# Optimization experiments

Measured on AMD Instinct MI355X. Metric: run time of the kernel, lower is better.

The kernel has to match this reference:

```python
import jax, jax.numpy as jnp
import numpy as np
import math

D = 128
LAMBDA_INIT = 0.8 - 0.6 * math.exp(-0.3 * 1)  # depth=1


def _clin(xr, xi, wr, wi, br, bi):
    # complex linear: (xr + i xi) @ (wr + i wi)^T + (br + i bi)
    o_r = jnp.einsum('bhsd,od->bhso', xr, wr) - jnp.einsum('bhsd,od->bhso', xi, wi) + br
    o_i = jnp.einsum('bhsd,od->bhso', xr, wi) + jnp.einsum('bhsd,od->bhso', xi, wr) + bi
    return o_r, o_i


def setup_inputs() -> dict:
    key = jax.random.key(0)
    ks = jax.random.split(key, 32)
    B, H, S = 1, 12, 1024
    shp = (B, H, S, D)
    inp = {}
    names = ['q_r', 'q_i', 'k_r', 'k_i', 'v_r', 'v_i', 'pe_q_r', 'pe_q_i', 'pe_k_r', 'pe_k_i']
    for i, n in enumerate(names):
        inp[n] = jax.random.normal(ks[i], shp, dtype=jnp.float32)
    std = 1.0 / math.sqrt(D)
    inp['qw_r'] = jax.random.normal(ks[10], (2 * D, D), jnp.float32) * std
    inp['qw_i'] = jax.random.normal(ks[11], (2 * D, D), jnp.float32) * std
    inp['qb_r'] = jnp.zeros((2 * D,), jnp.float32)
    inp['qb_i'] = jnp.zeros((2 * D,), jnp.float32)
    for j, p in enumerate(['k', 'v', 'g', 'o']):
        inp[p + 'w_r'] = jax.random.normal(ks[12 + 2 * j], (D, D), jnp.float32) * std
        inp[p + 'w_i'] = jax.random.normal(ks[13 + 2 * j], (D, D), jnp.float32) * std
        inp[p + 'b_r'] = jnp.zeros((D,), jnp.float32)
        inp[p + 'b_i'] = jnp.zeros((D,), jnp.float32)
    inp['lq1'] = jax.random.normal(ks[20], (D,), jnp.float32) * 0.1
    inp['lk1'] = jax.random.normal(ks[21], (D,), jnp.float32) * 0.1
    inp['lq2'] = jax.random.normal(ks[22], (D,), jnp.float32) * 0.1
    inp['lk2'] = jax.random.normal(ks[23], (D,), jnp.float32) * 0.1
    inp['sub_w'] = jnp.ones((2 * D,), jnp.float32)
    return inp


def _forward(q_r, q_i, k_r, k_i, v_r, v_i, pe_q_r, pe_q_i, pe_k_r, pe_k_i,
             qw_r, qw_i, qb_r, qb_i, kw_r, kw_i, kb_r, kb_i,
             vw_r, vw_i, vb_r, vb_i, gw_r, gw_i, gb_r, gb_i,
             ow_r, ow_i, ob_r, ob_i, lq1, lk1, lq2, lk2, sub_w):
    scale = D ** (-0.5)
    qp_r, qp_i = _clin(q_r, q_i, qw_r, qw_i, qb_r, qb_i)   # [B,H,S,2D]
    kp_r, kp_i = _clin(k_r, k_i, kw_r, kw_i, kb_r, kb_i)   # [B,H,S,D]
    vp_r, vp_i = _clin(v_r, v_i, vw_r, vw_i, vb_r, vb_i)
    qp_r = qp_r + jnp.concatenate([pe_q_r, pe_q_r], axis=-1)
    qp_i = qp_i + jnp.concatenate([pe_q_i, pe_q_i], axis=-1)
    kp_r = kp_r + pe_k_r
    kp_i = kp_i + pe_k_i
    q1_r, q2_r = jnp.split(qp_r, 2, axis=-1)
    q1_i, q2_i = jnp.split(qp_i, 2, axis=-1)

    def attn_w(qr, qi):
        s_r = jnp.einsum('bhqd,bhkd->bhqk', qr, kp_r) + jnp.einsum('bhqd,bhkd->bhqk', qi, kp_i)
        s_i = jnp.einsum('bhqd,bhkd->bhqk', qi, kp_r) - jnp.einsum('bhqd,bhkd->bhqk', qr, kp_i)
        mag = jnp.sqrt(s_r ** 2 + s_i ** 2 + 1e-8) * scale
        return jax.nn.softmax(mag.astype(jnp.float32), axis=-1).astype(s_r.dtype)

    w1 = attn_w(q1_r, q1_i)
    w2 = attn_w(q2_r, q2_i)
    a1_r = jnp.einsum('bhqk,bhkd->bhqd', w1, vp_r)
    a1_i = jnp.einsum('bhqk,bhkd->bhqd', w1, vp_i)
    a2_r = jnp.einsum('bhqk,bhkd->bhqd', w2, vp_r)
    a2_i = jnp.einsum('bhqk,bhkd->bhqd', w2, vp_i)
    cat_r = jnp.concatenate([a1_r, a2_r], axis=-1)
    cat_i = jnp.concatenate([a1_i, a2_i], axis=-1)
    rms = jnp.sqrt(jnp.mean(cat_r ** 2 + cat_i ** 2, axis=-1, keepdims=True) + 1e-5)
    cat_r = cat_r / rms * sub_w
    cat_i = cat_i / rms * sub_w
    a1_r, a2_r = jnp.split(cat_r, 2, axis=-1)
    a1_i, a2_i = jnp.split(cat_i, 2, axis=-1)
    lam1 = jnp.exp(jnp.sum(lq1 * lk1))
    lam2 = jnp.exp(jnp.sum(lq2 * lk2))
    lam = jax.nn.sigmoid(lam1 - lam2 + LAMBDA_INIT)
    out_r = a1_r - lam * a2_r
    out_i = a1_i - lam * a2_i
    g_r, g_i = _clin(q_r, q_i, gw_r, gw_i, gb_r, gb_i)
    out_r, out_i = g_r * out_r - g_i * out_i, g_r * out_i + g_i * out_r
    out_r, out_i = _clin(out_r, out_i, ow_r, ow_i, ob_r, ob_i)
    return out_r, out_i


def reference(q_r, q_i, k_r, k_i, v_r, v_i, pe_q_r, pe_q_i, pe_k_r, pe_k_i,
              qw_r, qw_i, qb_r, qb_i, kw_r, kw_i, kb_r, kb_i,
              vw_r, vw_i, vb_r, vb_i, gw_r, gw_i, gb_r, gb_i,
              ow_r, ow_i, ob_r, ob_i, lq1, lk1, lq2, lk2, sub_w):
    return _forward(q_r, q_i, k_r, k_i, v_r, v_i, pe_q_r, pe_q_i, pe_k_r, pe_k_i,
                    qw_r, qw_i, qb_r, qb_i, kw_r, kw_i, kb_r, kb_i,
                    vw_r, vw_i, vb_r, vb_i, gw_r, gw_i, gb_r, gb_i,
                    ow_r, ow_i, ob_r, ob_i, lq1, lk1, lq2, lk2, sub_w)
```

## Files before the change

### kernel.cpp

```cpp
#include <hip/hip_runtime.h>
#include <math.h>

#define H 12
#define S 1024
#define D 128
#define NROWS (H * S)

typedef __attribute__((ext_vector_type(8))) _Float16 f16x8;
typedef __attribute__((ext_vector_type(4))) float f32x4;
typedef __attribute__((ext_vector_type(4))) int i32x4;

__device__ __forceinline__ short f2h(float f) {
    _Float16 h = (_Float16)f;
    return __builtin_bit_cast(short, h);
}
__device__ __forceinline__ f16x8 fneg8(f16x8 v) {
    i32x4 u = __builtin_bit_cast(i32x4, v);
    u ^= (int)0x80008000;
    return __builtin_bit_cast(f16x8, u);
}

#define WS_QP_R   0ULL
#define WS_QP_I   6291456ULL
#define WS_KP_R   12582912ULL
#define WS_KP_I   15728640ULL
#define WS_VPT_R  18874368ULL
#define WS_VPT_I  22020096ULL
#define WS_G_R    25165824ULL
#define WS_G_I    31457280ULL
#define WS_ACAT_R 37748736ULL
#define WS_ACAT_I 50331648ULL
#define WS_LAM    62914560ULL
#define WS_SC     62914816ULL
#define W16_PER_HEAD  4194304ULL

__global__ void lam_kernel(const float* __restrict__ lq1, const float* __restrict__ lk1,
                           const float* __restrict__ lq2, const float* __restrict__ lk2,
                           float* __restrict__ lam_out)
{
    int t = threadIdx.x;
    float p1 = lq1[t] * lk1[t];
    float p2 = lq2[t] * lk2[t];
    #pragma unroll
    for (int off = 32; off; off >>= 1) {
        p1 += __shfl_xor(p1, off);
        p2 += __shfl_xor(p2, off);
    }
    __shared__ float s1[2], s2[2];
    if ((t & 63) == 0) { s1[t >> 6] = p1; s2[t >> 6] = p2; }
    __syncthreads();
    if (t == 0) {
        float l1 = expf(s1[0] + s1[1]);
        float l2 = expf(s2[0] + s2[1]);
        float x = l1 - l2 + 0.3555090675909693f;
        lam_out[0] = 1.0f / (1.0f + expf(-x));
    }
}

template <int OMODE>
__global__ __launch_bounds__(256) void clin_mfma(
    const float* __restrict__ xr, const float* __restrict__ xi,
    const float* __restrict__ wr, const float* __restrict__ wi,
    const float* __restrict__ br, const float* __restrict__ bi,
    const float* __restrict__ per, const float* __restrict__ pei,
    void* __restrict__ outr_, void* __restrict__ outi_, int M)
{
    __shared__ short As[64 * 72], Brs[64 * 72], Bis[64 * 72];
    const int t = threadIdx.x;
    const int row0 = blockIdx.x * 64, col0 = blockIdx.y * 64;
    const int lane = t & 63, wid = t >> 6;
    const int wm = (wid >> 1) * 32, wn = (wid & 1) * 32;
    const int fm = lane & 15, fq = lane >> 4;
    f32x4 zero4 = {0.f, 0.f, 0.f, 0.f};
    f32x4 accr[2][2], acci[2][2];
    #pragma unroll
    for (int i = 0; i < 2; ++i)
        #pragma unroll
        for (int j = 0; j < 2; ++j) { accr[i][j] = zero4; acci[i][j] = zero4; }

    for (int c = 0; c < 4; ++c) {
        const bool hi = (c >= 2);
        const int kb = (c & 1) * 64;
        const float* Asrc = hi ? xi : xr;
        const float* Brsrc = hi ? wi : wr;
        const float* Bisrc = hi ? wr : wi;
        const float bsign = hi ? -1.0f : 1.0f;
        __syncthreads();
        #pragma unroll
        for (int i = 0; i < 4; ++i) {
            int lin = i * 256 + t;
            int r = lin >> 4;
            int k4 = (lin & 15) * 4;
            float4 va = *(const float4*)&Asrc[(size_t)(row0 + r) * 128 + kb + k4];
            *(short4*)&As[r * 72 + k4] = make_short4(f2h(va.x), f2h(va.y), f2h(va.z), f2h(va.w));
            float4 vr = *(const float4*)&Brsrc[(size_t)(col0 + r) * 128 + kb + k4];
            *(short4*)&Brs[r * 72 + k4] = make_short4(f2h(bsign * vr.x), f2h(bsign * vr.y),
                                                      f2h(bsign * vr.z), f2h(bsign * vr.w));
            float4 vi = *(const float4*)&Bisrc[(size_t)(col0 + r) * 128 + kb + k4];
            *(short4*)&Bis[r * 72 + k4] = make_short4(f2h(vi.x), f2h(vi.y), f2h(vi.z), f2h(vi.w));
        }
        __syncthreads();
        #pragma unroll
        for (int ks = 0; ks < 64; ks += 32) {
            f16x8 a[2], bfr[2], bfi[2];
            #pragma unroll
            for (int i = 0; i < 2; ++i) {
                a[i]   = *(const f16x8*)&As[(wm + i * 16 + fm) * 72 + ks + fq * 8];
                bfr[i] = *(const f16x8*)&Brs[(wn + i * 16 + fm) * 72 + ks + fq * 8];
                bfi[i] = *(const f16x8*)&Bis[(wn + i * 16 + fm) * 72 + ks + fq * 8];
            }
            #pragma unroll
            for (int i = 0; i < 2; ++i)
                #pragma unroll
                for (int j = 0; j < 2; ++j) {
                    accr[i][j] = __builtin_amdgcn_mfma_f32_16x16x32_f16(a[i], bfr[j], accr[i][j], 0, 0, 0);
                    acci[i][j] = __builtin_amdgcn_mfma_f32_16x16x32_f16(a[i], bfi[j], acci[i][j], 0, 0, 0);
                }
        }
    }
    #pragma unroll
    for (int i = 0; i < 2; ++i)
        #pragma unroll
        for (int j = 0; j < 2; ++j) {
            int colc = col0 + wn + j * 16 + fm;
            float bbr = br[colc], bbi = bi[colc];
            if (OMODE == 2) {
                int rb = row0 + wm + i * 16 + fq * 4;
                int hq = rb >> 10, sq = rb & 1023;
                short4 o_r4, o_i4;
                float r0 = accr[i][j][0] + bbr, r1 = accr[i][j][1] + bbr;
                float r2 = accr[i][j][2] + bbr, r3 = accr[i][j][3] + bbr;
                float i0 = acci[i][j][0] + bbi, i1 = acci[i][j][1] + bbi;
                float i2v = acci[i][j][2] + bbi, i3 = acci[i][j][3] + bbi;
                o_r4 = make_short4(f2h(r0), f2h(r1), f2h(r2), f2h(r3));
                o_i4 = make_short4(f2h(i0), f2h(i1), f2h(i2v), f2h(i3));
                size_t ob = ((size_t)(hq * 128 + colc)) * 1024 + sq;
                *(short4*)&((short*)outr_)[ob] = o_r4;
                *(short4*)&((short*)outi_)[ob] = o_i4;
            } else {
                #pragma unroll
                for (int reg = 0; reg < 4; ++reg) {
                    int rr = row0 + wm + i * 16 + fq * 4 + reg;
                    float o_r = accr[i][j][reg] + bbr;
                    float o_i = acci[i][j][reg] + bbi;
                    if (per) {
                        o_r += per[(size_t)rr * 128 + (colc & 127)];
                        o_i += pei[(size_t)rr * 128 + (colc & 127)];
                    }
                    if (OMODE == 1) {
                        ((short*)outr_)[(size_t)rr * M + colc] = f2h(o_r);
                        ((short*)outi_)[(size_t)rr * M + colc] = f2h(o_i);
                    } else {
                        ((float*)outr_)[(size_t)rr * M + colc] = o_r;
                        ((float*)outi_)[(size_t)rr * M + colc] = o_i;
                    }
                }
            }
        }
}

__global__ __launch_bounds__(256) void score_mfma(
    const short* __restrict__ qp_r, const short* __restrict__ qp_i,
    const short* __restrict__ kp_r, const short* __restrict__ kp_i,
    short* __restrict__ w16, int h0)
{
    __shared__ short Qr[64 * 72], Qi[64 * 72], Kt[128 * 72];
    const int t = threadIdx.x;
    const int hh = blockIdx.z >> 1, map = blockIdx.z & 1;
    const int h = h0 + hh;
    const int q0 = blockIdx.x * 64, c0 = blockIdx.y * 128;
    const int lane = t & 63, wid = t >> 6;
    const int wm = (wid >> 1) * 32, wn = (wid & 1) * 64;
    const int fm = lane & 15, fq = lane >> 4;
    f32x4 zero4 = {0.f, 0.f, 0.f, 0.f};
    f32x4 sr[2][4], si[2][4];
    #pragma unroll
    for (int i = 0; i < 2; ++i)
        #pragma unroll
        for (int j = 0; j < 4; ++j) { sr[i][j] = zero4; si[i][j] = zero4; }

    for (int kb = 0; kb < 2; ++kb) {
        const int kbase = map * 128 + kb * 64;
        __syncthreads();
        #pragma unroll
        for (int i = 0; i < 4; ++i) {
            int lin = i * 256 + t;
            int r = lin >> 4, k4 = (lin & 15) * 4;
            size_t qb = (size_t)(h * S + q0 + r) * 256 + kbase + k4;
            *(short4*)&Qr[r * 72 + k4] = *(const short4*)&qp_r[qb];
            *(short4*)&Qi[r * 72 + k4] = *(const short4*)&qp_i[qb];
        }
        #pragma unroll
        for (int i = 0; i < 8; ++i) {
            int lin = i * 256 + t;
            int r = lin >> 4, k4 = (lin & 15) * 4;
            *(short4*)&Kt[r * 72 + k4] =
                *(const short4*)&kp_r[(size_t)(h * S + c0 + r) * 128 + kb * 64 + k4];
        }
        __syncthreads();
        f16x8 aR[2][2], aI[2][2];
        #pragma unroll
        for (int ks = 0; ks < 2; ++ks)
            #pragma unroll
            for (int i = 0; i < 2; ++i) {
                int ao = (wm + i * 16 + fm) * 72 + ks * 32 + fq * 8;
                aR[ks][i] = *(const f16x8*)&Qr[ao];
                aI[ks][i] = *(const f16x8*)&Qi[ao];
            }
        #pragma unroll
        for (int ks = 0; ks < 2; ++ks) {
            f16x8 b[4];
            #pragma unroll
            for (int j = 0; j < 4; ++j)
                b[j] = *(const f16x8*)&Kt[(wn + j * 16 + fm) * 72 + ks * 32 + fq * 8];
            #pragma unroll
            for (int i = 0; i < 2; ++i)
                #pragma unroll
                for (int j = 0; j < 4; ++j) {
                    sr[i][j] = __builtin_amdgcn_mfma_f32_16x16x32_f16(aR[ks][i], b[j], sr[i][j], 0, 0, 0);
                    si[i][j] = __builtin_amdgcn_mfma_f32_16x16x32_f16(aI[ks][i], b[j], si[i][j], 0, 0, 0);
                }
        }
        __syncthreads();
        #pragma unroll
        for (int i = 0; i < 8; ++i) {
            int lin = i * 256 + t;
            int r = lin >> 4, k4 = (lin & 15) * 4;
            *(short4*)&Kt[r * 72 + k4] =
                *(const short4*)&kp_i[(size_t)(h * S + c0 + r) * 128 + kb * 64 + k4];
        }
        __syncthreads();
        #pragma unroll
        for (int ks = 0; ks < 2; ++ks) {
            f16x8 b[4];
            #pragma unroll
            for (int j = 0; j < 4; ++j)
                b[j] = *(const f16x8*)&Kt[(wn + j * 16 + fm) * 72 + ks * 32 + fq * 8];
            f16x8 nR0 = fneg8(aR[ks][0]), nR1 = fneg8(aR[ks][1]);
            #pragma unroll
            for (int j = 0; j < 4; ++j) {
                sr[0][j] = __builtin_amdgcn_mfma_f32_16x16x32_f16(aI[ks][0], b[j], sr[0][j], 0, 0, 0);
                si[0][j] = __builtin_amdgcn_mfma_f32_16x16x32_f16(nR0, b[j], si[0][j], 0, 0, 0);
                sr[1][j] = __builtin_amdgcn_mfma_f32_16x16x32_f16(aI[ks][1], b[j], sr[1][j], 0, 0, 0);
                si[1][j] = __builtin_amdgcn_mfma_f32_16x16x32_f16(nR1, b[j], si[1][j], 0, 0, 0);
            }
        }
    }
    const float scale = 0.08838834764831845f;
    #pragma unroll
    for (int i = 0; i < 2; ++i)
        #pragma unroll
        for (int j = 0; j < 4; ++j) {
            int kcol = c0 + wn + j * 16 + fm;
            #pragma unroll
            for (int reg = 0; reg < 4; ++reg) {
                int q = q0 + wm + i * 16 + fq * 4 + reg;
                float r1 = sr[i][j][reg], I1 = si[i][j][reg];
                float m1 = sqrtf(fmaf(r1, r1, fmaf(I1, I1, 1e-8f))) * scale;
                w16[(((size_t)hh * 2 + map) * S + q) * S + kcol] = f2h(m1);
            }
        }
}

__global__ __launch_bounds__(256) void softmax_f16(short* __restrict__ w16)
{
    short* row = w16 + (size_t)blockIdx.x * S;
    int t = threadIdx.x;
    short4 s = ((short4*)row)[t];
    float f0 = (float)__builtin_bit_cast(_Float16, s.x);
    float f1 = (float)__builtin_bit_cast(_Float16, s.y);
    float f2v = (float)__builtin_bit_cast(_Float16, s.z);
    float f3 = (float)__builtin_bit_cast(_Float16, s.w);
    float m = fmaxf(fmaxf(f0, f1), fmaxf(f2v, f3));
    #pragma unroll
    for (int off = 32; off; off >>= 1) m = fmaxf(m, __shfl_xor(m, off));
    __shared__ float redm[4], reds[4];
    int w = t >> 6;
    if ((t & 63) == 0) redm[w] = m;
    __syncthreads();
    m = fmaxf(fmaxf(redm[0], redm[1]), fmaxf(redm[2], redm[3]));
    float e0 = __expf(f0 - m), e1 = __expf(f1 - m), e2 = __expf(f2v - m), e3 = __expf(f3 - m);
    float ssum = e0 + e1 + e2 + e3;
    #pragma unroll
    for (int off = 32; off; off >>= 1) ssum += __shfl_xor(ssum, off);
    if ((t & 63) == 0) reds[w] = ssum;
    __syncthreads();
    ssum = reds[0] + reds[1] + reds[2] + reds[3];
    float inv = 1.0f / ssum;
    s.x = f2h(e0 * inv); s.y = f2h(e1 * inv); s.z = f2h(e2 * inv); s.w = f2h(e3 * inv);
    ((short4*)row)[t] = s;
}

__global__ __launch_bounds__(256) void av_mfma(
    const short* __restrict__ w16, const short* __restrict__ vpT_r, const short* __restrict__ vpT_i,
    float* __restrict__ acat_r, float* __restrict__ acat_i, int h0)
{
    __shared__ short W1[64 * 72], W2[64 * 72], Vr[64 * 72], Vi[64 * 72];
    const int t = threadIdx.x;
    const int hh = blockIdx.z, h = h0 + hh;
    const int q0 = blockIdx.x * 64, d0 = blockIdx.y * 64;
    const int lane = t & 63, wid = t >> 6;
    const int wm = (wid >> 1) * 32, wn = (wid & 1) * 32;
    const int fm = lane & 15, fq = lane >> 4;
    f32x4 zero4 = {0.f, 0.f, 0.f, 0.f};
    f32x4 a1r[2][2], a1i[2][2], a2r[2][2], a2i[2][2];
    #pragma unroll
    for (int i = 0; i < 2; ++i)
        #pragma unroll
        for (int j = 0; j < 2; ++j) { a1r[i][j] = zero4; a1i[i][j] = zero4; a2r[i][j] = zero4; a2i[i][j] = zero4; }

    for (int k0 = 0; k0 < S; k0 += 64) {
        __syncthreads();
        #pragma unroll
        for (int i = 0; i < 4; ++i) {
            int lin = i * 256 + t;
            int r = lin >> 4, k4 = (lin & 15) * 4;
            *(short4*)&W1[r * 72 + k4] = *(const short4*)&w16[(((size_t)hh * 2 + 0) * S + q0 + r) * S + k0 + k4];
            *(short4*)&W2[r * 72 + k4] = *(const short4*)&w16[(((size_t)hh * 2 + 1) * S + q0 + r) * S + k0 + k4];
            size_t vb = (size_t)(h * 128 + d0 + r) * 1024 + k0 + k4;
            *(short4*)&Vr[r * 72 + k4] = *(const short4*)&vpT_r[vb];
            *(short4*)&Vi[r * 72 + k4] = *(const short4*)&vpT_i[vb];
        }
        __syncthreads();
        #pragma unroll
        for (int ks = 0; ks < 64; ks += 32) {
            f16x8 w1[2], w2[2], br[2], bi[2];
            #pragma unroll
            for (int i = 0; i < 2; ++i) {
                w1[i] = *(const f16x8*)&W1[(wm + i * 16 + fm) * 72 + ks + fq * 8];
                w2[i] = *(const f16x8*)&W2[(wm + i * 16 + fm) * 72 + ks + fq * 8];
                br[i] = *(const f16x8*)&Vr[(wn + i * 16 + fm) * 72 + ks + fq * 8];
                bi[i] = *(const f16x8*)&Vi[(wn + i * 16 + fm) * 72 + ks + fq * 8];
            }
            #pragma unroll
            for (int i = 0; i < 2; ++i)
                #pragma unroll
                for (int j = 0; j < 2; ++j) {
                    a1r[i][j] = __builtin_amdgcn_mfma_f32_16x16x32_f16(w1[i], br[j], a1r[i][j], 0, 0, 0);
                    a1i[i][j] = __builtin_amdgcn_mfma_f32_16x16x32_f16(w1[i], bi[j], a1i[i][j], 0, 0, 0);
                    a2r[i][j] = __builtin_amdgcn_mfma_f32_16x16x32_f16(w2[i], br[j], a2r[i][j], 0, 0, 0);
                    a2i[i][j] = __builtin_amdgcn_mfma_f32_16x16x32_f16(w2[i], bi[j], a2i[i][j], 0, 0, 0);
                }
        }
    }
    #pragma unroll
    for (int i = 0; i < 2; ++i)
        #pragma unroll
        for (int j = 0; j < 2; ++j) {
            int d = d0 + wn + j * 16 + fm;
            #pragma unroll
            for (int reg = 0; reg < 4; ++reg) {
                int q = q0 + wm + i * 16 + fq * 4 + reg;
                size_t rowb = (size_t)(h * S + q) * 256;
                acat_r[rowb + d]       = a1r[i][j][reg];
                acat_r[rowb + 128 + d] = a2r[i][j][reg];
                acat_i[rowb + d]       = a1i[i][j][reg];
                acat_i[rowb + 128 + d] = a2i[i][j][reg];
            }
        }
}

__global__ __launch_bounds__(256) void rmsgate_kernel(
    const float* __restrict__ acat_r, const float* __restrict__ acat_i,
    const float* __restrict__ sub_w, const float* __restrict__ lam_ptr,
    float* __restrict__ g_r, float* __restrict__ g_i)
{
    int row = blockIdx.x;
    int t = threadIdx.x;
    float ar = acat_r[(size_t)row * 256 + t];
    float ai = acat_i[(size_t)row * 256 + t];
    float ss = fmaf(ar, ar, ai * ai);
    #pragma unroll
    for (int off = 32; off; off >>= 1) ss += __shfl_xor(ss, off);
    __shared__ float red[4];
    if ((t & 63) == 0) red[t >> 6] = ss;
    __syncthreads();
    float total = red[0] + red[1] + red[2] + red[3];
    float inv_rms = 1.0f / sqrtf(total * (1.0f / 256.0f) + 1e-5f);
    float sw = sub_w[t];
    __shared__ float Cr[256], Ci[256];
    Cr[t] = ar * inv_rms * sw;
    Ci[t] = ai * inv_rms * sw;
    __syncthreads();
    if (t < 128) {
        float lam = lam_ptr[0];
        float o_r = Cr[t] - lam * Cr[t + 128];
        float o_i = Ci[t] - lam * Ci[t + 128];
        float gr = g_r[(size_t)row * 128 + t];
        float gi = g_i[(size_t)row * 128 + t];
        g_r[(size_t)row * 128 + t] = gr * o_r - gi * o_i;
        g_i[(size_t)row * 128 + t] = gr * o_i + gi * o_r;
    }
}

extern "C" void kernel_launch(void* const* d_in, const int* in_sizes, int n_in,
                              void* d_out, int out_size, void* d_ws, size_t ws_size,
                              hipStream_t stream)
{
    (void)in_sizes; (void)n_in; (void)out_size;
    const float* q_r    = (const float*)d_in[0];
    const float* q_i    = (const float*)d_in[1];
    const float* k_r    = (const float*)d_in[2];
    const float* k_i    = (const float*)d_in[3];
    const float* v_r    = (const float*)d_in[4];
    const float* v_i    = (const float*)d_in[5];
    const float* pe_q_r = (const float*)d_in[6];
    const float* pe_q_i = (const float*)d_in[7];
    const float* pe_k_r = (const float*)d_in[8];
    const float* pe_k_i = (const float*)d_in[9];
    const float* qw_r   = (const float*)d_in[10];
    const float* qw_i   = (const float*)d_in[11];
    const float* qb_r   = (const float*)d_in[12];
    const float* qb_i   = (const float*)d_in[13];
    const float* kw_r   = (const float*)d_in[14];
    const float* kw_i   = (const float*)d_in[15];
    const float* kb_r   = (const float*)d_in[16];
    const float* kb_i   = (const float*)d_in[17];
    const float* vw_r   = (const float*)d_in[18];
    const float* vw_i   = (const float*)d_in[19];
    const float* vb_r   = (const float*)d_in[20];
    const float* vb_i   = (const float*)d_in[21];
    const float* gw_r   = (const float*)d_in[22];
    const float* gw_i   = (const float*)d_in[23];
    const float* gb_r   = (const float*)d_in[24];
    const float* gb_i   = (const float*)d_in[25];
    const float* ow_r   = (const float*)d_in[26];
    const float* ow_i   = (const float*)d_in[27];
    const float* ob_r   = (const float*)d_in[28];
    const float* ob_i   = (const float*)d_in[29];
    const float* lq1    = (const float*)d_in[30];
    const float* lk1    = (const float*)d_in[31];
    const float* lq2    = (const float*)d_in[32];
    const float* lk2    = (const float*)d_in[33];
    const float* sub_w  = (const float*)d_in[34];

    char* ws = (char*)d_ws;
    short* qp_r   = (short*)(ws + WS_QP_R);
    short* qp_i   = (short*)(ws + WS_QP_I);
    short* kp_r   = (short*)(ws + WS_KP_R);
    short* kp_i   = (short*)(ws + WS_KP_I);
    short* vpT_r  = (short*)(ws + WS_VPT_R);
    short* vpT_i  = (short*)(ws + WS_VPT_I);
    float* g_r    = (float*)(ws + WS_G_R);
    float* g_i    = (float*)(ws + WS_G_I);
    float* acat_r = (float*)(ws + WS_ACAT_R);
    float* acat_i = (float*)(ws + WS_ACAT_I);
    float* lam    = (float*)(ws + WS_LAM);
    short* w16    = (short*)(ws + WS_SC);

    float* out_r = (float*)d_out;
    float* out_i = out_r + (size_t)NROWS * D;

    size_t avail = ws_size > WS_SC ? ws_size - WS_SC : 0;
    int nh_chunk = (int)(avail / W16_PER_HEAD);
    if (nh_chunk < 1) nh_chunk = 1;
    if (nh_chunk > H) nh_chunk = H;

    lam_kernel<<<1, 128, 0, stream>>>(lq1, lk1, lq2, lk2, lam);

    clin_mfma<1><<<dim3(192, 4), 256, 0, stream>>>(q_r, q_i, qw_r, qw_i, qb_r, qb_i,
                                                   pe_q_r, pe_q_i, qp_r, qp_i, 256);
    clin_mfma<1><<<dim3(192, 2), 256, 0, stream>>>(k_r, k_i, kw_r, kw_i, kb_r, kb_i,
                                                   pe_k_r, pe_k_i, kp_r, kp_i, 128);
    clin_mfma<2><<<dim3(192, 2), 256, 0, stream>>>(v_r, v_i, vw_r, vw_i, vb_r, vb_i,
                                                   nullptr, nullptr, vpT_r, vpT_i, 128);
    clin_mfma<0><<<dim3(192, 2), 256, 0, stream>>>(q_r, q_i, gw_r, gw_i, gb_r, gb_i,
                                                   nullptr, nullptr, g_r, g_i, 128);

    for (int h0 = 0; h0 < H; h0 += nh_chunk) {
        int nhh = (H - h0 < nh_chunk) ? (H - h0) : nh_chunk;
        score_mfma<<<dim3(16, 8, nhh * 2), 256, 0, stream>>>(qp_r, qp_i, kp_r, kp_i, w16, h0);
        softmax_f16<<<nhh * 2 * S, 256, 0, stream>>>(w16);
        av_mfma<<<dim3(16, 2, nhh), 256, 0, stream>>>(w16, vpT_r, vpT_i, acat_r, acat_i, h0);
    }

    rmsgate_kernel<<<NROWS, 256, 0, stream>>>(acat_r, acat_i, sub_w, lam, g_r, g_i);

    clin_mfma<0><<<dim3(192, 2), 256, 0, stream>>>(g_r, g_i, ow_r, ow_i, ob_r, ob_i,
                                                   nullptr, nullptr, out_r, out_i, 128);
}
```

Measured before the change: 320.1 us.

## Enlarge GEMM tiles and split AV kernel by complex component

The complex-linear and score kernels now use 128-row M tiles with 4x2 and 4x4 per-wave fragment grids. This halves the grid size and raises reuse of the shared B/K tile. The AV kernel now handles one complex component per block across all 128 output dims, so each W tile is reused across 128 columns, but the W tiles are loaded twice, once per component. The larger tiles use more registers and LDS, which can lower occupancy, and the smaller grids (96 or 192 blocks) may underfill the GPU's 256 CUs.

```diff
diff --git a/kernel.cpp b/kernel.cpp
--- a/kernel.cpp
+++ b/kernel.cpp
@@ -65,16 +65,16 @@
     const float* __restrict__ per, const float* __restrict__ pei,
     void* __restrict__ outr_, void* __restrict__ outi_, int M)
 {
-    __shared__ short As[64 * 72], Brs[64 * 72], Bis[64 * 72];
+    __shared__ short As[128 * 72], Brs[64 * 72], Bis[64 * 72];
     const int t = threadIdx.x;
-    const int row0 = blockIdx.x * 64, col0 = blockIdx.y * 64;
+    const int row0 = blockIdx.x * 128, col0 = blockIdx.y * 64;
     const int lane = t & 63, wid = t >> 6;
-    const int wm = (wid >> 1) * 32, wn = (wid & 1) * 32;
+    const int wm = (wid >> 1) * 64, wn = (wid & 1) * 32;
     const int fm = lane & 15, fq = lane >> 4;
     f32x4 zero4 = {0.f, 0.f, 0.f, 0.f};
-    f32x4 accr[2][2], acci[2][2];
-    #pragma unroll
-    for (int i = 0; i < 2; ++i)
+    f32x4 accr[4][2], acci[4][2];
+    #pragma unroll
+    for (int i = 0; i < 4; ++i)
         #pragma unroll
         for (int j = 0; j < 2; ++j) { accr[i][j] = zero4; acci[i][j] = zero4; }
 
@@ -87,12 +87,16 @@
         const float bsign = hi ? -1.0f : 1.0f;
         __syncthreads();
         #pragma unroll
-        for (int i = 0; i < 4; ++i) {
-            int lin = i * 256 + t;
-            int r = lin >> 4;
-            int k4 = (lin & 15) * 4;
+        for (int it = 0; it < 8; ++it) {
+            int lin = it * 256 + t;
+            int r = lin >> 4, k4 = (lin & 15) * 4;
             float4 va = *(const float4*)&Asrc[(size_t)(row0 + r) * 128 + kb + k4];
             *(short4*)&As[r * 72 + k4] = make_short4(f2h(va.x), f2h(va.y), f2h(va.z), f2h(va.w));
+        }
+        #pragma unroll
+        for (int it = 0; it < 4; ++it) {
+            int lin = it * 256 + t;
+            int r = lin >> 4, k4 = (lin & 15) * 4;
             float4 vr = *(const float4*)&Brsrc[(size_t)(col0 + r) * 128 + kb + k4];
             *(short4*)&Brs[r * 72 + k4] = make_short4(f2h(bsign * vr.x), f2h(bsign * vr.y),
                                                       f2h(bsign * vr.z), f2h(bsign * vr.w));
@@ -102,24 +106,25 @@
         __syncthreads();
         #pragma unroll
         for (int ks = 0; ks < 64; ks += 32) {
-            f16x8 a[2], bfr[2], bfi[2];
-            #pragma unroll
-            for (int i = 0; i < 2; ++i) {
-                a[i]   = *(const f16x8*)&As[(wm + i * 16 + fm) * 72 + ks + fq * 8];
-                bfr[i] = *(const f16x8*)&Brs[(wn + i * 16 + fm) * 72 + ks + fq * 8];
-                bfi[i] = *(const f16x8*)&Bis[(wn + i * 16 + fm) * 72 + ks + fq * 8];
-            }
-            #pragma unroll
-            for (int i = 0; i < 2; ++i)
+            f16x8 bfr[2], bfi[2];
+            #pragma unroll
+            for (int j = 0; j < 2; ++j) {
+                bfr[j] = *(const f16x8*)&Brs[(wn + j * 16 + fm) * 72 + ks + fq * 8];
+                bfi[j] = *(const f16x8*)&Bis[(wn + j * 16 + fm) * 72 + ks + fq * 8];
+            }
+            #pragma unroll
+            for (int i = 0; i < 4; ++i) {
+                f16x8 a = *(const f16x8*)&As[(wm + i * 16 + fm) * 72 + ks + fq * 8];
                 #pragma unroll
                 for (int j = 0; j < 2; ++j) {
-                    accr[i][j] = __builtin_amdgcn_mfma_f32_16x16x32_f16(a[i], bfr[j], accr[i][j], 0, 0, 0);
-                    acci[i][j] = __builtin_amdgcn_mfma_f32_16x16x32_f16(a[i], bfi[j], acci[i][j], 0, 0, 0);
+                    accr[i][j] = __builtin_amdgcn_mfma_f32_16x16x32_f16(a, bfr[j], accr[i][j], 0, 0, 0);
+                    acci[i][j] = __builtin_amdgcn_mfma_f32_16x16x32_f16(a, bfi[j], acci[i][j], 0, 0, 0);
                 }
-        }
-    }
-    #pragma unroll
-    for (int i = 0; i < 2; ++i)
+            }
+        }
+    }
+    #pragma unroll
+    for (int i = 0; i < 4; ++i)
         #pragma unroll
         for (int j = 0; j < 2; ++j) {
             int colc = col0 + wn + j * 16 + fm;
@@ -127,13 +132,10 @@
             if (OMODE == 2) {
                 int rb = row0 + wm + i * 16 + fq * 4;
                 int hq = rb >> 10, sq = rb & 1023;
-                short4 o_r4, o_i4;
-                float r0 = accr[i][j][0] + bbr, r1 = accr[i][j][1] + bbr;
-                float r2 = accr[i][j][2] + bbr, r3 = accr[i][j][3] + bbr;
-                float i0 = acci[i][j][0] + bbi, i1 = acci[i][j][1] + bbi;
-                float i2v = acci[i][j][2] + bbi, i3 = acci[i][j][3] + bbi;
-                o_r4 = make_short4(f2h(r0), f2h(r1), f2h(r2), f2h(r3));
-                o_i4 = make_short4(f2h(i0), f2h(i1), f2h(i2v), f2h(i3));
+                short4 o_r4 = make_short4(f2h(accr[i][j][0] + bbr), f2h(accr[i][j][1] + bbr),
+                                          f2h(accr[i][j][2] + bbr), f2h(accr[i][j][3] + bbr));
+                short4 o_i4 = make_short4(f2h(acci[i][j][0] + bbi), f2h(acci[i][j][1] + bbi),
+                                          f2h(acci[i][j][2] + bbi), f2h(acci[i][j][3] + bbi));
                 size_t ob = ((size_t)(hq * 128 + colc)) * 1024 + sq;
                 *(short4*)&((short*)outr_)[ob] = o_r4;
                 *(short4*)&((short*)outi_)[ob] = o_i4;
@@ -164,18 +166,18 @@
     const short* __restrict__ kp_r, const short* __restrict__ kp_i,
     short* __restrict__ w16, int h0)
 {
-    __shared__ short Qr[64 * 72], Qi[64 * 72], Kt[128 * 72];
+    __shared__ short Qr[128 * 72], Qi[128 * 72], Kt[128 * 72];
     const int t = threadIdx.x;
     const int hh = blockIdx.z >> 1, map = blockIdx.z & 1;
     const int h = h0 + hh;
-    const int q0 = blockIdx.x * 64, c0 = blockIdx.y * 128;
+    const int q0 = blockIdx.x * 128, c0 = blockIdx.y * 128;
     const int lane = t & 63, wid = t >> 6;
-    const int wm = (wid >> 1) * 32, wn = (wid & 1) * 64;
+    const int wm = (wid >> 1) * 64, wn = (wid & 1) * 64;
     const int fm = lane & 15, fq = lane >> 4;
     f32x4 zero4 = {0.f, 0.f, 0.f, 0.f};
-    f32x4 sr[2][4], si[2][4];
-    #pragma unroll
-    for (int i = 0; i < 2; ++i)
+    f32x4 sr[4][4], si[4][4];
+    #pragma unroll
+    for (int i = 0; i < 4; ++i)
         #pragma unroll
         for (int j = 0; j < 4; ++j) { sr[i][j] = zero4; si[i][j] = zero4; }
 
@@ -183,72 +185,66 @@
         const int kbase = map * 128 + kb * 64;
         __syncthreads();
         #pragma unroll
-        for (int i = 0; i < 4; ++i) {
-            int lin = i * 256 + t;
+        for (int it = 0; it < 8; ++it) {
+            int lin = it * 256 + t;
             int r = lin >> 4, k4 = (lin & 15) * 4;
             size_t qb = (size_t)(h * S + q0 + r) * 256 + kbase + k4;
             *(short4*)&Qr[r * 72 + k4] = *(const short4*)&qp_r[qb];
             *(short4*)&Qi[r * 72 + k4] = *(const short4*)&qp_i[qb];
-        }
-        #pragma unroll
-        for (int i = 0; i < 8; ++i) {
-            int lin = i * 256 + t;
-            int r = lin >> 4, k4 = (lin & 15) * 4;
             *(short4*)&Kt[r * 72 + k4] =
                 *(const short4*)&kp_r[(size_t)(h * S + c0 + r) * 128 + kb * 64 + k4];
         }
         __syncthreads();
-        f16x8 aR[2][2], aI[2][2];
-        #pragma unroll
-        for (int ks = 0; ks < 2; ++ks)
-            #pragma unroll
-            for (int i = 0; i < 2; ++i) {
-                int ao = (wm + i * 16 + fm) * 72 + ks * 32 + fq * 8;
-                aR[ks][i] = *(const f16x8*)&Qr[ao];
-                aI[ks][i] = *(const f16x8*)&Qi[ao];
-            }
-        #pragma unroll
-        for (int ks = 0; ks < 2; ++ks) {
+        #pragma unroll
+        for (int ks = 0; ks < 64; ks += 32) {
             f16x8 b[4];
             #pragma unroll
             for (int j = 0; j < 4; ++j)
-                b[j] = *(const f16x8*)&Kt[(wn + j * 16 + fm) * 72 + ks * 32 + fq * 8];
-            #pragma unroll
-            for (int i = 0; i < 2; ++i)
+                b[j] = *(const f16x8*)&Kt[(wn + j * 16 + fm) * 72 + ks + fq * 8];
+            #pragma unroll
+            for (int i = 0; i < 4; ++i) {
+                int ao = (wm + i * 16 + fm) * 72 + ks + fq * 8;
+                f16x8 ar = *(const f16x8*)&Qr[ao];
+                f16x8 ai = *(const f16x8*)&Qi[ao];
                 #pragma unroll
                 for (int j = 0; j < 4; ++j) {
-                    sr[i][j] = __builtin_amdgcn_mfma_f32_16x16x32_f16(aR[ks][i], b[j], sr[i][j], 0, 0, 0);
-                    si[i][j] = __builtin_amdgcn_mfma_f32_16x16x32_f16(aI[ks][i], b[j], si[i][j], 0, 0, 0);
+                    sr[i][j] = __builtin_amdgcn_mfma_f32_16x16x32_f16(ar, b[j], sr[i][j], 0, 0, 0);
+                    si[i][j] = __builtin_amdgcn_mfma_f32_16x16x32_f16(ai, b[j], si[i][j], 0, 0, 0);
                 }
-        }
-        __syncthreads();
-        #pragma unroll
-        for (int i = 0; i < 8; ++i) {
-            int lin = i * 256 + t;
+            }
+        }
+        __syncthreads();
+        #pragma unroll
+        for (int it = 0; it < 8; ++it) {
+            int lin = it * 256 + t;
             int r = lin >> 4, k4 = (lin & 15) * 4;
             *(short4*)&Kt[r * 72 + k4] =
                 *(const short4*)&kp_i[(size_t)(h * S + c0 + r) * 128 + kb * 64 + k4];
         }
         __syncthreads();
         #pragma unroll
-        for (int ks = 0; ks < 2; ++ks) {
+        for (int ks = 0; ks < 64; ks += 32) {
             f16x8 b[4];
             #pragma unroll
             for (int j = 0; j < 4; ++j)
-                b[j] = *(const f16x8*)&Kt[(wn + j * 16 + fm) * 72 + ks * 32 + fq * 8];
-            f16x8 nR0 = fneg8(aR[ks][0]), nR1 = fneg8(aR[ks][1]);
-            #pragma unroll
-            for (int j = 0; j < 4; ++j) {
-                sr[0][j] = __builtin_amdgcn_mfma_f32_16x16x32_f16(aI[ks][0], b[j], sr[0][j], 0, 0, 0);
-                si[0][j] = __builtin_amdgcn_mfma_f32_16x16x32_f16(nR0, b[j], si[0][j], 0, 0, 0);
-                sr[1][j] = __builtin_amdgcn_mfma_f32_16x16x32_f16(aI[ks][1], b[j], sr[1][j], 0, 0, 0);
-                si[1][j] = __builtin_amdgcn_mfma_f32_16x16x32_f16(nR1, b[j], si[1][j], 0, 0, 0);
+                b[j] = *(const f16x8*)&Kt[(wn + j * 16 + fm) * 72 + ks + fq * 8];
+            #pragma unroll
+            for (int i = 0; i < 4; ++i) {
+                int ao = (wm + i * 16 + fm) * 72 + ks + fq * 8;
+                f16x8 ar = *(const f16x8*)&Qr[ao];
+                f16x8 ai = *(const f16x8*)&Qi[ao];
+                f16x8 nr = fneg8(ar);
+                #pragma unroll
+                for (int j = 0; j < 4; ++j) {
+                    sr[i][j] = __builtin_amdgcn_mfma_f32_16x16x32_f16(ai, b[j], sr[i][j], 0, 0, 0);
+                    si[i][j] = __builtin_amdgcn_mfma_f32_16x16x32_f16(nr, b[j], si[i][j], 0, 0, 0);
+                }
             }
         }
     }
     const float scale = 0.08838834764831845f;
     #pragma unroll
-    for (int i = 0; i < 2; ++i)
+    for (int i = 0; i < 4; ++i)
         #pragma unroll
         for (int j = 0; j < 4; ++j) {
             int kcol = c0 + wn + j * 16 + fm;
@@ -295,67 +291,69 @@
     const short* __restrict__ w16, const short* __restrict__ vpT_r, const short* __restrict__ vpT_i,
     float* __restrict__ acat_r, float* __restrict__ acat_i, int h0)
 {
-    __shared__ short W1[64 * 72], W2[64 * 72], Vr[64 * 72], Vi[64 * 72];
+    __shared__ short W1[64 * 72], W2[64 * 72], Vc[128 * 72];
     const int t = threadIdx.x;
     const int hh = blockIdx.z, h = h0 + hh;
-    const int q0 = blockIdx.x * 64, d0 = blockIdx.y * 64;
+    const int comp = blockIdx.y;
+    const int q0 = blockIdx.x * 64;
+    const short* vpT = comp ? vpT_i : vpT_r;
+    float* acat = comp ? acat_i : acat_r;
     const int lane = t & 63, wid = t >> 6;
-    const int wm = (wid >> 1) * 32, wn = (wid & 1) * 32;
+    const int wm = (wid >> 1) * 32, wn = (wid & 1) * 64;
     const int fm = lane & 15, fq = lane >> 4;
     f32x4 zero4 = {0.f, 0.f, 0.f, 0.f};
-    f32x4 a1r[2][2], a1i[2][2], a2r[2][2], a2i[2][2];
+    f32x4 a1[2][4], a2[2][4];
     #pragma unroll
     for (int i = 0; i < 2; ++i)
         #pragma unroll
-        for (int j = 0; j < 2; ++j) { a1r[i][j] = zero4; a1i[i][j] = zero4; a2r[i][j] = zero4; a2i[i][j] = zero4; }
+        for (int j = 0; j < 4; ++j) { a1[i][j] = zero4; a2[i][j] = zero4; }
 
     for (int k0 = 0; k0 < S; k0 += 64) {
         __syncthreads();
         #pragma unroll
-        for (int i = 0; i < 4; ++i) {
-            int lin = i * 256 + t;
+        for (int it = 0; it < 4; ++it) {
+            int lin = it * 256 + t;
             int r = lin >> 4, k4 = (lin & 15) * 4;
             *(short4*)&W1[r * 72 + k4] = *(const short4*)&w16[(((size_t)hh * 2 + 0) * S + q0 + r) * S + k0 + k4];
             *(short4*)&W2[r * 72 + k4] = *(const short4*)&w16[(((size_t)hh * 2 + 1) * S + q0 + r) * S + k0 + k4];
-            size_t vb = (size_t)(h * 128 + d0 + r) * 1024 + k0 + k4;
-            *(short4*)&Vr[r * 72 + k4] = *(const short4*)&vpT_r[vb];
-            *(short4*)&Vi[r * 72 + k4] = *(const short4*)&vpT_i[vb];
+        }
+        #pragma unroll
+        for (int it = 0; it < 8; ++it) {
+            int lin = it * 256 + t;
+            int dd = lin >> 4, k4 = (lin & 15) * 4;
+            *(short4*)&Vc[dd * 72 + k4] = *(const short4*)&vpT[(size_t)(h * 128 + dd) * 1024 + k0 + k4];
         }
         __syncthreads();
         #pragma unroll
         for (int ks = 0; ks < 64; ks += 32) {
-            f16x8 w1[2], w2[2], br[2], bi[2];
+            f16x8 b[4];
+            #pragma unroll
+            for (int j = 0; j < 4; ++j)
+                b[j] = *(const f16x8*)&Vc[(wn + j * 16 + fm) * 72 + ks + fq * 8];
             #pragma unroll
             for (int i = 0; i < 2; ++i) {
-                w1[i] = *(const f16x8*)&W1[(wm + i * 16 + fm) * 72 + ks + fq * 8];
-                w2[i] = *(const f16x8*)&W2[(wm + i * 16 + fm) * 72 + ks + fq * 8];
-                br[i] = *(const f16x8*)&Vr[(wn + i * 16 + fm) * 72 + ks + fq * 8];
-                bi[i] = *(const f16x8*)&Vi[(wn + i * 16 + fm) * 72 + ks + fq * 8];
-            }
-            #pragma unroll
-            for (int i = 0; i < 2; ++i)
+                int wo = (wm + i * 16 + fm) * 72 + ks + fq * 8;
+                f16x8 w1f = *(const f16x8*)&W1[wo];
+                f16x8 w2f = *(const f16x8*)&W2[wo];
                 #pragma unroll
-                for (int j = 0; j < 2; ++j) {
-                    a1r[i][j] = __builtin_amdgcn_mfma_f32_16x16x32_f16(w1[i], br[j], a1r[i][j], 0, 0, 0);
-                    a1i[i][j] = __builtin_amdgcn_mfma_f32_16x16x32_f16(w1[i], bi[j], a1i[i][j], 0, 0, 0);
-                    a2r[i][j] = __builtin_amdgcn_mfma_f32_16x16x32_f16(w2[i], br[j], a2r[i][j], 0, 0, 0);
-                    a2i[i][j] = __builtin_amdgcn_mfma_f32_16x16x32_f16(w2[i], bi[j], a2i[i][j], 0, 0, 0);
+                for (int j = 0; j < 4; ++j) {
+                    a1[i][j] = __builtin_amdgcn_mfma_f32_16x16x32_f16(w1f, b[j], a1[i][j], 0, 0, 0);
+                    a2[i][j] = __builtin_amdgcn_mfma_f32_16x16x32_f16(w2f, b[j], a2[i][j], 0, 0, 0);
                 }
+            }
         }
     }
     #pragma unroll
     for (int i = 0; i < 2; ++i)
         #pragma unroll
-        for (int j = 0; j < 2; ++j) {
-            int d = d0 + wn + j * 16 + fm;
+        for (int j = 0; j < 4; ++j) {
+            int d = wn + j * 16 + fm;
             #pragma unroll
             for (int reg = 0; reg < 4; ++reg) {
                 int q = q0 + wm + i * 16 + fq * 4 + reg;
                 size_t rowb = (size_t)(h * S + q) * 256;
-                acat_r[rowb + d]       = a1r[i][j][reg];
-                acat_r[rowb + 128 + d] = a2r[i][j][reg];
-                acat_i[rowb + d]       = a1i[i][j][reg];
-                acat_i[rowb + 128 + d] = a2i[i][j][reg];
+                acat[rowb + d]       = a1[i][j][reg];
+                acat[rowb + 128 + d] = a2[i][j][reg];
             }
         }
 }
@@ -458,24 +456,24 @@
 
     lam_kernel<<<1, 128, 0, stream>>>(lq1, lk1, lq2, lk2, lam);
 
-    clin_mfma<1><<<dim3(192, 4), 256, 0, stream>>>(q_r, q_i, qw_r, qw_i, qb_r, qb_i,
-                                                   pe_q_r, pe_q_i, qp_r, qp_i, 256);
-    clin_mfma<1><<<dim3(192, 2), 256, 0, stream>>>(k_r, k_i, kw_r, kw_i, kb_r, kb_i,
-                                                   pe_k_r, pe_k_i, kp_r, kp_i, 128);
-    clin_mfma<2><<<dim3(192, 2), 256, 0, stream>>>(v_r, v_i, vw_r, vw_i, vb_r, vb_i,
-                                                   nullptr, nullptr, vpT_r, vpT_i, 128);
-    clin_mfma<0><<<dim3(192, 2), 256, 0, stream>>>(q_r, q_i, gw_r, gw_i, gb_r, gb_i,
-                                                   nullptr, nullptr, g_r, g_i, 128);
+    clin_mfma<1><<<dim3(96, 4), 256, 0, stream>>>(q_r, q_i, qw_r, qw_i, qb_r, qb_i,
+                                                  pe_q_r, pe_q_i, qp_r, qp_i, 256);
+    clin_mfma<1><<<dim3(96, 2), 256, 0, stream>>>(k_r, k_i, kw_r, kw_i, kb_r, kb_i,
+                                                  pe_k_r, pe_k_i, kp_r, kp_i, 128);
+    clin_mfma<2><<<dim3(96, 2), 256, 0, stream>>>(v_r, v_i, vw_r, vw_i, vb_r, vb_i,
+                                                  nullptr, nullptr, vpT_r, vpT_i, 128);
+    clin_mfma<0><<<dim3(96, 2), 256, 0, stream>>>(q_r, q_i, gw_r, gw_i, gb_r, gb_i,
+                                                  nullptr, nullptr, g_r, g_i, 128);
 
     for (int h0 = 0; h0 < H; h0 += nh_chunk) {
         int nhh = (H - h0 < nh_chunk) ? (H - h0) : nh_chunk;
-        score_mfma<<<dim3(16, 8, nhh * 2), 256, 0, stream>>>(qp_r, qp_i, kp_r, kp_i, w16, h0);
+        score_mfma<<<dim3(8, 8, nhh * 2), 256, 0, stream>>>(qp_r, qp_i, kp_r, kp_i, w16, h0);
         softmax_f16<<<nhh * 2 * S, 256, 0, stream>>>(w16);
         av_mfma<<<dim3(16, 2, nhh), 256, 0, stream>>>(w16, vpT_r, vpT_i, acat_r, acat_i, h0);
     }
 
     rmsgate_kernel<<<NROWS, 256, 0, stream>>>(acat_r, acat_i, sub_w, lam, g_r, g_i);
 
-    clin_mfma<0><<<dim3(192, 2), 256, 0, stream>>>(g_r, g_i, ow_r, ow_i, ob_r, ob_i,
-                                                   nullptr, nullptr, out_r, out_i, 128);
-}
+    clin_mfma<0><<<dim3(96, 2), 256, 0, stream>>>(g_r, g_i, ow_r, ow_i, ob_r, ob_i,
+                                                  nullptr, nullptr, out_r, out_i, 128);
+}
```

Measured after the change: 349.0 us. +9.1%, slower.
